# Optimization experiments

Hardware: AMD Instinct MI355X
Metric: run time of the kernel (lower is better)

Reference implementation:

```python
import math
import jax, jax.numpy as jnp
import numpy as np

L, D, H, DF, V, T, B = 4, 1024, 16, 4096, 32000, 2048, 1
HD = D // H
EPS = 1e-5

def _ln(x, w, b):
    m = jnp.mean(x, -1, keepdims=True)
    v = jnp.mean((x - m) ** 2, -1, keepdims=True)
    return (x - m) * jax.lax.rsqrt(v + EPS) * w + b

def setup_inputs() -> dict:
    key = jax.random.key(0)
    ks = jax.random.split(key, 8)
    s = 0.02
    return {
        'ids':   jax.random.randint(ks[0], (B, T), 0, V),
        'te':    jax.random.normal(ks[1], (V, D), jnp.float32) * s,
        'pe':    jax.random.normal(ks[2], (T, D), jnp.float32) * s,
        'qkv_w': jax.random.normal(ks[3], (L, D, 3 * D), jnp.float32) * s,
        'qkv_b': jnp.zeros((L, 3 * D), jnp.float32),
        'out_w': jax.random.normal(ks[4], (L, D, D), jnp.float32) * s,
        'out_b': jnp.zeros((L, D), jnp.float32),
        'ln1_w': jnp.ones((L, D), jnp.float32),
        'ln1_b': jnp.zeros((L, D), jnp.float32),
        'ln2_w': jnp.ones((L, D), jnp.float32),
        'ln2_b': jnp.zeros((L, D), jnp.float32),
        'up_w':  jax.random.normal(ks[5], (L, D, DF), jnp.float32) * s,
        'up_b':  jnp.zeros((L, DF), jnp.float32),
        'dn_w':  jax.random.normal(ks[6], (L, DF, D), jnp.float32) * s,
        'dn_b':  jnp.zeros((L, D), jnp.float32),
        'lnf_w': jnp.ones((D,), jnp.float32),
        'lnf_b': jnp.zeros((D,), jnp.float32),
    }

def reference(ids, te, pe, qkv_w, qkv_b, out_w, out_b, ln1_w, ln1_b,
              ln2_w, ln2_b, up_w, up_b, dn_w, dn_b, lnf_w, lnf_b):
    b, t = ids.shape
    x = te[ids] + pe[:t][None]                        # [b,t,D]
    causal = jnp.tril(jnp.ones((t, t), bool))          # [t,t]
    scale = 1.0 / math.sqrt(HD)
    for i in range(L):
        h = _ln(x, ln1_w[i], ln1_b[i])
        qkv = (h @ qkv_w[i] + qkv_b[i]).reshape(b, t, 3, H, HD)
        q, k, v = qkv[:, :, 0], qkv[:, :, 1], qkv[:, :, 2]
        sc = jnp.einsum('bqhd,bkhd->bhqk', q, k) * scale
        sc = jnp.where(causal, sc, -jnp.inf)
        att = jax.nn.softmax(sc, axis=-1)
        ao = jnp.einsum('bhqk,bkhd->bqhd', att, v).reshape(b, t, D)
        x = x + ao @ out_w[i] + out_b[i]
        h = _ln(x, ln2_w[i], ln2_b[i])
        x = x + jax.nn.silu(h @ up_w[i] + up_b[i]) @ dn_w[i] + dn_b[i]
    x = _ln(x, lnf_w, lnf_b)
    logits = x @ te.T                                  # tied head, no bias
    return logits
```

## Files before the change

kernel.cpp:

```cpp
#include <hip/hip_runtime.h>

typedef __attribute__((ext_vector_type(8))) short short8;
typedef __attribute__((ext_vector_type(4))) short short4v;
typedef __attribute__((ext_vector_type(4))) float f32x4;
typedef unsigned short u16;

#define Lc 4
#define Dc 1024
#define Hc 16
#define HDc 64
#define DFc 4096
#define Vc 32000
#define Tc 2048

__device__ __forceinline__ u16 f2bf(float f) {
  union { float f; unsigned u; } v; v.f = f;
  return (u16)((v.u + 0x7FFFu + ((v.u >> 16) & 1u)) >> 16);
}

__device__ __forceinline__ void gload_lds16(const u16* g, u16* l) {
  __builtin_amdgcn_global_load_lds(
      (const __attribute__((address_space(1))) unsigned int*)(g),
      (__attribute__((address_space(3))) unsigned int*)(l), 16, 0, 0);
}

#define BARS do { __builtin_amdgcn_s_barrier(); __builtin_amdgcn_sched_barrier(0); } while (0)
#define LGKM0 do { asm volatile("s_waitcnt lgkmcnt(0)" ::: "memory"); __builtin_amdgcn_sched_barrier(0); } while (0)
#define VMC(n) do { asm volatile("s_waitcnt vmcnt(" #n ")" ::: "memory"); __builtin_amdgcn_sched_barrier(0); } while (0)

__global__ __launch_bounds__(256) void castk(const float* __restrict__ in, u16* __restrict__ out) {
  size_t i = ((size_t)blockIdx.x * 256 + threadIdx.x) * 4;
  float4 v = *(const float4*)(in + i);
  short4v o; o[0] = f2bf(v.x); o[1] = f2bf(v.y); o[2] = f2bf(v.z); o[3] = f2bf(v.w);
  *(short4v*)(out + i) = o;
}

__global__ __launch_bounds__(256) void embedln(const int* __restrict__ ids, const float* __restrict__ te,
                                               const float* __restrict__ pe, const float* __restrict__ w,
                                               const float* __restrict__ b, float* __restrict__ x,
                                               u16* __restrict__ out) {
  int t = blockIdx.x, tid = threadIdx.x;
  int id = ids[t];
  float4 a = *(const float4*)(te + (size_t)id * Dc + tid * 4);
  float4 p = *(const float4*)(pe + (size_t)t * Dc + tid * 4);
  float4 v; v.x = a.x + p.x; v.y = a.y + p.y; v.z = a.z + p.z; v.w = a.w + p.w;
  size_t i = (size_t)t * Dc + tid * 4;
  *(float4*)(x + i) = v;
  float s = v.x + v.y + v.z + v.w;
  float q = v.x * v.x + v.y * v.y + v.z * v.z + v.w * v.w;
  #pragma unroll
  for (int off = 1; off < 64; off <<= 1) { s += __shfl_xor(s, off); q += __shfl_xor(q, off); }
  __shared__ float red[8];
  if ((tid & 63) == 0) { red[tid >> 6] = s; red[4 + (tid >> 6)] = q; }
  __syncthreads();
  s = red[0] + red[1] + red[2] + red[3];
  q = red[4] + red[5] + red[6] + red[7];
  float mean = s * (1.0f / Dc);
  float rstd = rsqrtf(q * (1.0f / Dc) - mean * mean + 1e-5f);
  float4 wv = *(const float4*)(w + tid * 4);
  float4 bv = *(const float4*)(b + tid * 4);
  out[i + 0] = f2bf((v.x - mean) * rstd * wv.x + bv.x);
  out[i + 1] = f2bf((v.y - mean) * rstd * wv.y + bv.y);
  out[i + 2] = f2bf((v.z - mean) * rstd * wv.z + bv.z);
  out[i + 3] = f2bf((v.w - mean) * rstd * wv.w + bv.w);
}

template<int SK>
__global__ __launch_bounds__(256) void combineln(float* __restrict__ x, const float* __restrict__ p,
                                                 const float* __restrict__ bias, const float* __restrict__ w,
                                                 const float* __restrict__ b, u16* __restrict__ out) {
  int t = blockIdx.x, tid = threadIdx.x;
  size_t i = (size_t)t * Dc + tid * 4;
  float4 v = *(const float4*)(x + i);
  #pragma unroll
  for (int s = 0; s < SK; s++) {
    float4 q2 = *(const float4*)(p + (size_t)s * Tc * Dc + i);
    v.x += q2.x; v.y += q2.y; v.z += q2.z; v.w += q2.w;
  }
  float4 bb = *(const float4*)(bias + tid * 4);
  v.x += bb.x; v.y += bb.y; v.z += bb.z; v.w += bb.w;
  *(float4*)(x + i) = v;
  float s = v.x + v.y + v.z + v.w;
  float q = v.x * v.x + v.y * v.y + v.z * v.z + v.w * v.w;
  #pragma unroll
  for (int off = 1; off < 64; off <<= 1) { s += __shfl_xor(s, off); q += __shfl_xor(q, off); }
  __shared__ float red[8];
  if ((tid & 63) == 0) { red[tid >> 6] = s; red[4 + (tid >> 6)] = q; }
  __syncthreads();
  s = red[0] + red[1] + red[2] + red[3];
  q = red[4] + red[5] + red[6] + red[7];
  float mean = s * (1.0f / Dc);
  float rstd = rsqrtf(q * (1.0f / Dc) - mean * mean + 1e-5f);
  float4 wv = *(const float4*)(w + tid * 4);
  float4 bv = *(const float4*)(b + tid * 4);
  out[i + 0] = f2bf((v.x - mean) * rstd * wv.x + bv.x);
  out[i + 1] = f2bf((v.y - mean) * rstd * wv.y + bv.y);
  out[i + 2] = f2bf((v.z - mean) * rstd * wv.z + bv.z);
  out[i + 3] = f2bf((v.w - mean) * rstd * wv.w + bv.w);
}

__global__ __launch_bounds__(256) void transpose4(const float* __restrict__ qw, const float* __restrict__ ow,
                                                  const float* __restrict__ uw, const float* __restrict__ dw,
                                                  u16* __restrict__ qT, u16* __restrict__ oT,
                                                  u16* __restrict__ uT, u16* __restrict__ dT) {
  __shared__ float tl[32][33];
  int id = blockIdx.x;
  const float* in; u16* out; int R, C, t;
  if (id < 3072)      { in = qw; out = qT; R = Dc;  C = 3 * Dc; t = id; }
  else if (id < 4096) { in = ow; out = oT; R = Dc;  C = Dc;     t = id - 3072; }
  else if (id < 8192) { in = uw; out = uT; R = Dc;  C = DFc;    t = id - 4096; }
  else                { in = dw; out = dT; R = DFc; C = Dc;     t = id - 8192; }
  int tilesX = C >> 5;
  int c0 = (t % tilesX) * 32, r0 = (t / tilesX) * 32;
  int lx = threadIdx.x & 31, ly = threadIdx.x >> 5;
  #pragma unroll
  for (int i = ly; i < 32; i += 8) tl[i][lx] = in[(size_t)(r0 + i) * C + c0 + lx];
  __syncthreads();
  #pragma unroll
  for (int i = ly; i < 32; i += 8) out[(size_t)(c0 + i) * R + r0 + lx] = f2bf(tl[lx][i]);
}

template<int EPI>
__global__ __launch_bounds__(256) void gemm128m(
    const u16* __restrict__ A, const u16* __restrict__ Bt, const float* __restrict__ bias,
    u16* __restrict__ outb, float* __restrict__ outf, int M, int N, int K, int KS) {
  __shared__ __align__(16) u16 lds[32768];
  u16* As = lds;
  u16* Bs = lds + 16384;
  const int NK = KS >> 6;

  int tid = threadIdx.x;
  int w = tid >> 6, lane = tid & 63;
  int lr = lane & 15, lg = lane >> 4;
  int wr = w >> 1, wc = w & 1;

  int m0 = blockIdx.y * 128, n0 = blockIdx.x * 128;
  int kbase = blockIdx.z * KS;

  int offg[4];
  #pragma unroll
  for (int j = 0; j < 4; j++) {
    int p = tid + j * 256;
    int row = p >> 3;
    int uc = (p & 7) ^ (row & 7);
    offg[j] = row * K + uc * 8;
  }
  const u16* aB = A + (size_t)m0 * K + kbase;
  const u16* bB = Bt + (size_t)n0 * K + kbase;

  auto stA = [&](int kt) {
    u16* l = As + ((kt & 1) << 13) + w * 512;
    #pragma unroll
    for (int j = 0; j < 4; j++)
      gload_lds16(aB + kt * 64 + offg[j], l + j * 2048);
  };
  auto stB = [&](int kt) {
    u16* l = Bs + ((kt & 1) << 13) + w * 512;
    #pragma unroll
    for (int j = 0; j < 4; j++)
      gload_lds16(bB + kt * 64 + offg[j], l + j * 2048);
  };

  int colx0 = ((0 * 4 + lg) ^ (lr & 7)) * 8;
  int colx1 = ((1 * 4 + lg) ^ (lr & 7)) * 8;
  int abase = (wr * 64 + lr) * 64;
  int bbase = (wc * 64 + lr) * 64;

  f32x4 acc[4][4] = {};

  stB(0); stA(0); stB(1);
  VMC(4);
  BARS;

  for (int kt = 0; kt < NK; ++kt) {
    const u16* sA = As + ((kt & 1) << 13);
    const u16* sB = Bs + ((kt & 1) << 13);
    short8 af[4][2], bf[4][2];

    #pragma unroll
    for (int m = 0; m < 2; m++) {
      af[m][0] = *(const short8*)(sA + abase + m * 1024 + colx0);
      af[m][1] = *(const short8*)(sA + abase + m * 1024 + colx1);
    }
    #pragma unroll
    for (int n = 0; n < 4; n++) {
      bf[n][0] = *(const short8*)(sB + bbase + n * 1024 + colx0);
      bf[n][1] = *(const short8*)(sB + bbase + n * 1024 + colx1);
    }
    if (kt + 1 < NK) stA(kt + 1);
    BARS;
    LGKM0;
    __builtin_amdgcn_s_setprio(1);
    #pragma unroll
    for (int m = 0; m < 2; m++)
      #pragma unroll
      for (int n = 0; n < 4; n++)
        #pragma unroll
        for (int ks = 0; ks < 2; ks++)
          acc[m][n] = __builtin_amdgcn_mfma_f32_16x16x32_bf16(af[m][ks], bf[n][ks], acc[m][n], 0, 0, 0);
    __builtin_amdgcn_s_setprio(0);
    BARS;

    #pragma unroll
    for (int m = 2; m < 4; m++) {
      af[m][0] = *(const short8*)(sA + abase + m * 1024 + colx0);
      af[m][1] = *(const short8*)(sA + abase + m * 1024 + colx1);
    }
    if (kt + 2 < NK) { stB(kt + 2); VMC(4); }
    else if (kt + 1 < NK) { VMC(0); }
    BARS;
    LGKM0;
    __builtin_amdgcn_s_setprio(1);
    #pragma unroll
    for (int m = 2; m < 4; m++)
      #pragma unroll
      for (int n = 0; n < 4; n++)
        #pragma unroll
        for (int ks = 0; ks < 2; ks++)
          acc[m][n] = __builtin_amdgcn_mfma_f32_16x16x32_bf16(af[m][ks], bf[n][ks], acc[m][n], 0, 0, 0);
    __builtin_amdgcn_s_setprio(0);
    BARS;
  }

  float* op = outf + (EPI == 4 ? (size_t)blockIdx.z * M * N : 0);
  u16* vtp = (u16*)outf;
  #pragma unroll
  for (int n = 0; n < 4; n++) {
    int gn = n0 + wc * 64 + n * 16 + lr;
    float bv = (EPI == 0 || EPI == 1 || EPI == 5) ? bias[gn] : 0.0f;
    #pragma unroll
    for (int m = 0; m < 4; m++) {
      if (EPI == 5 && gn >= 2 * Dc) {
        int gmb = m0 + wr * 64 + m * 16 + lg * 4;
        short4v o;
        #pragma unroll
        for (int r = 0; r < 4; r++) o[r] = (short)f2bf(acc[m][n][r] + bv);
        *(short4v*)(vtp + (size_t)(gn - 2 * Dc) * Tc + gmb) = o;
      } else {
        #pragma unroll
        for (int r = 0; r < 4; r++) {
          int gm = m0 + wr * 64 + m * 16 + lg * 4 + r;
          float v = acc[m][n][r] + bv;
          size_t idx = (size_t)gm * N + gn;
          if (EPI == 0 || EPI == 5) outb[idx] = f2bf(v);
          else if (EPI == 1) outb[idx] = f2bf(v / (1.0f + __expf(-v)));
          else op[idx] = v;
        }
      }
    }
  }
}

__global__ __launch_bounds__(512) void gemm256(const u16* __restrict__ A, const u16* __restrict__ Bt,
                                               float* __restrict__ outf, int M, int N, int K) {
  __shared__ __align__(16) u16 lds[65536];
  u16* AsU = lds;
  u16* BsU = lds + 32768;
  const int NK = K >> 6;

  int tid = threadIdx.x;
  int w = tid >> 6, lane = tid & 63;
  int lr = lane & 15, lg = lane >> 4;
  int wr = w >> 2, wc = w & 3;

  int flat = blockIdx.y * gridDim.x + blockIdx.x;
  {
    int nwg = gridDim.x * gridDim.y;
    int q = nwg >> 3, r = nwg & 7, xc = flat & 7, s = flat >> 3;
    flat = (xc < r ? xc * (q + 1) : r * (q + 1) + (xc - r) * q) + s;
  }
  int bm = flat % gridDim.x, bn = flat / gridDim.x;
  int m0 = bm * 256, n0 = bn * 256;

  int row0 = tid >> 3;
  int uc0 = (tid & 7) ^ (row0 & 7);
  int offg = row0 * K + uc0 * 8;
  const u16* aB = A + (size_t)m0 * K;
  const u16* bB = Bt + (size_t)n0 * K;

  auto stA = [&](int kt, int half) {
    const u16* g = aB + (size_t)half * 128 * K + kt * 64 + offg;
    u16* l = AsU + (((kt & 1) * 2 + half) << 13) + w * 512;
    gload_lds16(g, l);
    gload_lds16(g + 64 * K, l + 4096);
  };
  auto stB = [&](int kt, int half) {
    const u16* g = bB + (size_t)half * 128 * K + kt * 64 + offg;
    u16* l = BsU + (((kt & 1) * 2 + half) << 13) + w * 512;
    gload_lds16(g, l);
    gload_lds16(g + 64 * K, l + 4096);
  };

  int colx0 = ((0 * 4 + lg) ^ (lr & 7)) * 8;
  int colx1 = ((1 * 4 + lg) ^ (lr & 7)) * 8;
  int arow = lr * 64;
  int brow = ((wc & 1) * 64 + lr) * 64;

  f32x4 acc[8][4] = {};

  stB(0, 0); stB(0, 1); stA(0, 0); stA(0, 1); stB(1, 0); stB(1, 1);
  VMC(4);
  BARS;

  for (int kt = 0; kt < NK; ++kt) {
    int slot = kt & 1;
    const u16* sA = AsU + ((slot * 2 + wr) << 13);
    const u16* sB = BsU + ((slot * 2 + (wc >> 1)) << 13);
    short8 af0[4][2], af1[4][2], bf0[2][2], bf1[2][2];

    #pragma unroll
    for (int m = 0; m < 4; m++) {
      af0[m][0] = *(const short8*)(sA + arow + m * 1024 + colx0);
      af0[m][1] = *(const short8*)(sA + arow + m * 1024 + colx1);
    }
    #pragma unroll
    for (int n = 0; n < 2; n++) {
      bf0[n][0] = *(const short8*)(sB + brow + n * 1024 + colx0);
      bf0[n][1] = *(const short8*)(sB + brow + n * 1024 + colx1);
      bf1[n][0] = *(const short8*)(sB + brow + (n + 2) * 1024 + colx0);
      bf1[n][1] = *(const short8*)(sB + brow + (n + 2) * 1024 + colx1);
    }
    if (kt + 1 < NK) { stA(kt + 1, 0); stA(kt + 1, 1); }
    BARS;
    LGKM0;
    __builtin_amdgcn_s_setprio(1);
    #pragma unroll
    for (int m = 0; m < 4; m++)
      #pragma unroll
      for (int n = 0; n < 2; n++)
        #pragma unroll
        for (int ks = 0; ks < 2; ks++)
          acc[m][n] = __builtin_amdgcn_mfma_f32_16x16x32_bf16(af0[m][ks], bf0[n][ks], acc[m][n], 0, 0, 0);
    #pragma unroll
    for (int m = 0; m < 4; m++)
      #pragma unroll
      for (int n = 0; n < 2; n++)
        #pragma unroll
        for (int ks = 0; ks < 2; ks++)
          acc[m][n + 2] = __builtin_amdgcn_mfma_f32_16x16x32_bf16(af0[m][ks], bf1[n][ks], acc[m][n + 2], 0, 0, 0);
    __builtin_amdgcn_s_setprio(0);
    BARS;

    #pragma unroll
    for (int m = 0; m < 4; m++) {
      af1[m][0] = *(const short8*)(sA + arow + (m + 4) * 1024 + colx0);
      af1[m][1] = *(const short8*)(sA + arow + (m + 4) * 1024 + colx1);
    }
    if (kt + 2 < NK) { stB(kt + 2, 0); stB(kt + 2, 1); VMC(4); }
    else if (kt + 1 < NK) { VMC(0); }
    BARS;
    LGKM0;
    __builtin_amdgcn_s_setprio(1);
    #pragma unroll
    for (int m = 0; m < 4; m++)
      #pragma unroll
      for (int n = 0; n < 2; n++)
        #pragma unroll
        for (int ks = 0; ks < 2; ks++)
          acc[m + 4][n] = __builtin_amdgcn_mfma_f32_16x16x32_bf16(af1[m][ks], bf0[n][ks], acc[m + 4][n], 0, 0, 0);
    #pragma unroll
    for (int m = 0; m < 4; m++)
      #pragma unroll
      for (int n = 0; n < 2; n++)
        #pragma unroll
        for (int ks = 0; ks < 2; ks++)
          acc[m + 4][n + 2] = __builtin_amdgcn_mfma_f32_16x16x32_bf16(af1[m][ks], bf1[n][ks], acc[m + 4][n + 2], 0, 0, 0);
    __builtin_amdgcn_s_setprio(0);
    BARS;
  }

  #pragma unroll
  for (int m = 0; m < 8; m++) {
    #pragma unroll
    for (int n = 0; n < 4; n++) {
      int gn = n0 + wc * 64 + n * 16 + lr;
      #pragma unroll
      for (int r = 0; r < 4; r++) {
        int gm = m0 + wr * 128 + m * 16 + lg * 4 + r;
        outf[(size_t)gm * N + gn] = acc[m][n][r];
      }
    }
  }
}

__global__ __launch_bounds__(512) void attnk(const u16* __restrict__ qkv, const u16* __restrict__ vt,
                                             u16* __restrict__ ao) {
  __shared__ u16 Plds[8][16][72];
  __shared__ float Cacc[4][64][16];
  __shared__ float Cl[4][64][4];
  int bid = blockIdx.x;
  int hh = bid >> 5;
  int qb = (bid & 256) ? (31 - (bid & 31)) : (bid & 31);
  int tid = threadIdx.x, l = tid & 63, w = tid >> 6;
  int w4 = w & 3, ishi = w >> 2;
  int lr = l & 15, lg = l >> 4;
  int qr0 = qb * 64 + w4 * 16;
  const u16* qbase = qkv + (size_t)(qr0 + lr) * (3 * Dc) + hh * HDc + lg * 8;
  short8 aq0 = *(const short8*)qbase;
  short8 aq1 = *(const short8*)(qbase + 32);
  f32x4 acco[4] = {};
  float rs[4] = {0.0f, 0.0f, 0.0f, 0.0f};
  int nkb = (qr0 + 79) >> 6;
  int half = nkb >> 1;
  int klo = ishi ? half : 0;
  int khi = ishi ? nkb : half;
  const float cl2 = 0.125f * 1.44269504088896f;
  for (int kb = klo; kb < khi; kb++) {
    int kk0 = kb * 64;
    float sv[4][4];
    bool msk = (kb == nkb - 1);
    #pragma unroll
    for (int st = 0; st < 4; st++) {
      int kt0 = kk0 + st * 16;
      const u16* kbase = qkv + (size_t)(kt0 + lr) * (3 * Dc) + Dc + hh * HDc + lg * 8;
      short8 bk0 = *(const short8*)kbase;
      short8 bk1 = *(const short8*)(kbase + 32);
      f32x4 s = {};
      s = __builtin_amdgcn_mfma_f32_16x16x32_bf16(aq0, bk0, s, 0, 0, 0);
      s = __builtin_amdgcn_mfma_f32_16x16x32_bf16(aq1, bk1, s, 0, 0, 0);
      if (msk) {
        int gcol = kt0 + lr;
        #pragma unroll
        for (int r = 0; r < 4; r++) {
          int grow = qr0 + lg * 4 + r;
          sv[st][r] = (gcol <= grow) ? s[r] * cl2 : -__builtin_inff();
        }
      } else {
        #pragma unroll
        for (int r = 0; r < 4; r++) sv[st][r] = s[r] * cl2;
      }
    }
    #pragma unroll
    for (int st = 0; st < 4; st++) {
      #pragma unroll
      for (int r = 0; r < 4; r++) {
        float p = __builtin_amdgcn_exp2f(fminf(sv[st][r], 45.0f));
        sv[st][r] = p;
        rs[r] += p;
      }
    }
    #pragma unroll
    for (int st = 0; st < 4; st++) {
      #pragma unroll
      for (int r = 0; r < 4; r++) Plds[w][lg * 4 + r][st * 16 + lr] = f2bf(sv[st][r]);
    }
    short8 pa0 = *(const short8*)&Plds[w][lr][lg * 8];
    short8 pa1 = *(const short8*)&Plds[w][lr][32 + lg * 8];
    #pragma unroll
    for (int nt = 0; nt < 4; nt++) {
      const u16* vbase = vt + (size_t)(hh * HDc + nt * 16 + lr) * Tc + kk0 + lg * 8;
      short8 bv0 = *(const short8*)vbase;
      short8 bv1 = *(const short8*)(vbase + 32);
      acco[nt] = __builtin_amdgcn_mfma_f32_16x16x32_bf16(pa0, bv0, acco[nt], 0, 0, 0);
      acco[nt] = __builtin_amdgcn_mfma_f32_16x16x32_bf16(pa1, bv1, acco[nt], 0, 0, 0);
    }
  }
  #pragma unroll
  for (int off = 1; off < 16; off <<= 1) {
    #pragma unroll
    for (int r = 0; r < 4; r++) rs[r] += __shfl_xor(rs[r], off);
  }
  if (ishi) {
    #pragma unroll
    for (int nt = 0; nt < 4; nt++)
      #pragma unroll
      for (int r = 0; r < 4; r++) Cacc[w4][l][nt * 4 + r] = acco[nt][r];
    #pragma unroll
    for (int r = 0; r < 4; r++) Cl[w4][l][r] = rs[r];
  }
  __syncthreads();
  if (!ishi) {
    float linv[4];
    #pragma unroll
    for (int r = 0; r < 4; r++) linv[r] = 1.0f / (rs[r] + Cl[w4][l][r]);
    #pragma unroll
    for (int nt = 0; nt < 4; nt++) {
      #pragma unroll
      for (int r = 0; r < 4; r++) {
        float val = (acco[nt][r] + Cacc[w4][l][nt * 4 + r]) * linv[r];
        ao[(size_t)(qr0 + lg * 4 + r) * Dc + hh * HDc + nt * 16 + lr] = f2bf(val);
      }
    }
  }
}

extern "C" void kernel_launch(void* const* d_in, const int* in_sizes, int n_in,
                              void* d_out, int out_size, void* d_ws, size_t ws_size,
                              hipStream_t stream) {
  const int*   ids   = (const int*)d_in[0];
  const float* te    = (const float*)d_in[1];
  const float* pe    = (const float*)d_in[2];
  const float* qkv_w = (const float*)d_in[3];
  const float* qkv_b = (const float*)d_in[4];
  const float* out_w = (const float*)d_in[5];
  const float* out_b = (const float*)d_in[6];
  const float* ln1_w = (const float*)d_in[7];
  const float* ln1_b = (const float*)d_in[8];
  const float* ln2_w = (const float*)d_in[9];
  const float* ln2_b = (const float*)d_in[10];
  const float* up_w  = (const float*)d_in[11];
  const float* up_b  = (const float*)d_in[12];
  const float* dn_w  = (const float*)d_in[13];
  const float* dn_b  = (const float*)d_in[14];
  const float* lnf_w = (const float*)d_in[15];
  const float* lnf_b = (const float*)d_in[16];
  float* logits = (float*)d_out;

  char* ws = (char*)d_ws;
  size_t off = 0;
  auto alloc = [&](size_t bytes) { void* p = ws + off; off += (bytes + 255) & ~(size_t)255; return p; };
  float* x    = (float*)alloc((size_t)Tc * Dc * 4);
  u16* hbuf   = (u16*)alloc((size_t)Tc * Dc * 2);
  u16* qkvb   = (u16*)alloc((size_t)Tc * 3 * Dc * 2);
  u16* aob    = (u16*)alloc((size_t)Tc * Dc * 2);
  u16* ubuf   = (u16*)alloc((size_t)Tc * DFc * 2);
  u16* vtb    = (u16*)alloc((size_t)Dc * Tc * 2);
  u16* tebf   = (u16*)alloc((size_t)Vc * Dc * 2);
  u16* qkvT   = (u16*)alloc((size_t)3 * Dc * Dc * 2);
  u16* outT   = (u16*)alloc((size_t)Dc * Dc * 2);
  u16* upT    = (u16*)alloc((size_t)DFc * Dc * 2);
  u16* dnT    = (u16*)alloc((size_t)Dc * DFc * 2);
  float* pbuf = (float*)alloc((size_t)4 * Tc * Dc * 4);

  castk<<<Vc * Dc / 1024, 256, 0, stream>>>(te, tebf);
  embedln<<<Tc, 256, 0, stream>>>(ids, te, pe, ln1_w, ln1_b, x, hbuf);

  for (int i = 0; i < Lc; i++) {
    transpose4<<<12288, 256, 0, stream>>>(
        qkv_w + (size_t)i * Dc * 3 * Dc, out_w + (size_t)i * Dc * Dc,
        up_w + (size_t)i * Dc * DFc, dn_w + (size_t)i * DFc * Dc,
        qkvT, outT, upT, dnT);

    gemm128m<5><<<dim3(3 * Dc / 128, Tc / 128, 1), 256, 0, stream>>>(
        hbuf, qkvT, qkv_b + (size_t)i * 3 * Dc, qkvb, (float*)vtb, Tc, 3 * Dc, Dc, Dc);
    attnk<<<512, 512, 0, stream>>>(qkvb, vtb, aob);
    gemm128m<4><<<dim3(Dc / 128, Tc / 128, 2), 256, 0, stream>>>(
        aob, outT, nullptr, nullptr, pbuf, Tc, Dc, Dc, Dc / 2);
    combineln<2><<<Tc, 256, 0, stream>>>(x, pbuf, out_b + (size_t)i * Dc,
                                         ln2_w + (size_t)i * Dc, ln2_b + (size_t)i * Dc, hbuf);
    gemm128m<1><<<dim3(DFc / 128, Tc / 128, 1), 256, 0, stream>>>(
        hbuf, upT, up_b + (size_t)i * DFc, ubuf, nullptr, Tc, DFc, Dc, Dc);
    gemm128m<4><<<dim3(Dc / 128, Tc / 128, 4), 256, 0, stream>>>(
        ubuf, dnT, nullptr, nullptr, pbuf, Tc, Dc, DFc, DFc / 4);
    if (i < Lc - 1)
      combineln<4><<<Tc, 256, 0, stream>>>(x, pbuf, dn_b + (size_t)i * Dc,
                                           ln1_w + (size_t)(i + 1) * Dc, ln1_b + (size_t)(i + 1) * Dc, hbuf);
    else
      combineln<4><<<Tc, 256, 0, stream>>>(x, pbuf, dn_b + (size_t)i * Dc, lnf_w, lnf_b, hbuf);
  }

  gemm256<<<dim3(Tc / 256, Vc / 256), 512, 0, stream>>>(hbuf, tebf, logits, Tc, Vc, Dc);
}
```

Baseline: 938.7 us.

## Prefetch LDS fragments across phases and stage logits epilogue through LDS

```diff
diff --git a/kernel.cpp b/kernel.cpp
--- a/kernel.cpp
+++ b/kernel.cpp
@@ -25,7 +25,7 @@
 }
 
 #define BARS do { __builtin_amdgcn_s_barrier(); __builtin_amdgcn_sched_barrier(0); } while (0)
-#define LGKM0 do { asm volatile("s_waitcnt lgkmcnt(0)" ::: "memory"); __builtin_amdgcn_sched_barrier(0); } while (0)
+#define LGKM(n) do { asm volatile("s_waitcnt lgkmcnt(" #n ")" ::: "memory"); __builtin_amdgcn_sched_barrier(0); } while (0)
 #define VMC(n) do { asm volatile("s_waitcnt vmcnt(" #n ")" ::: "memory"); __builtin_amdgcn_sched_barrier(0); } while (0)
 
 __global__ __launch_bounds__(256) void castk(const float* __restrict__ in, u16* __restrict__ out) {
@@ -189,7 +189,7 @@
     }
     if (kt + 1 < NK) stA(kt + 1);
     BARS;
-    LGKM0;
+    LGKM(0);
     __builtin_amdgcn_s_setprio(1);
     #pragma unroll
     for (int m = 0; m < 2; m++)
@@ -209,7 +209,7 @@
     if (kt + 2 < NK) { stB(kt + 2); VMC(4); }
     else if (kt + 1 < NK) { VMC(0); }
     BARS;
-    LGKM0;
+    LGKM(0);
     __builtin_amdgcn_s_setprio(1);
     #pragma unroll
     for (int m = 2; m < 4; m++)
@@ -296,23 +296,26 @@
   int arow = lr * 64;
   int brow = ((wc & 1) * 64 + lr) * 64;
 
-  f32x4 acc[8][4] = {};
-
-  stB(0, 0); stB(0, 1); stA(0, 0); stA(0, 1); stB(1, 0); stB(1, 1);
-  VMC(4);
-  BARS;
-
-  for (int kt = 0; kt < NK; ++kt) {
-    int slot = kt & 1;
+  short8 af0[4][2], af1[4][2], bf0[2][2], bf1[2][2];
+
+  auto rd_af_lo = [&](int slot) {
     const u16* sA = AsU + ((slot * 2 + wr) << 13);
-    const u16* sB = BsU + ((slot * 2 + (wc >> 1)) << 13);
-    short8 af0[4][2], af1[4][2], bf0[2][2], bf1[2][2];
-
     #pragma unroll
     for (int m = 0; m < 4; m++) {
       af0[m][0] = *(const short8*)(sA + arow + m * 1024 + colx0);
       af0[m][1] = *(const short8*)(sA + arow + m * 1024 + colx1);
     }
+  };
+  auto rd_af_hi = [&](int slot) {
+    const u16* sA = AsU + ((slot * 2 + wr) << 13);
+    #pragma unroll
+    for (int m = 0; m < 4; m++) {
+      af1[m][0] = *(const short8*)(sA + arow + (m + 4) * 1024 + colx0);
+      af1[m][1] = *(const short8*)(sA + arow + (m + 4) * 1024 + colx1);
+    }
+  };
+  auto rd_bf = [&](int slot) {
+    const u16* sB = BsU + ((slot * 2 + (wc >> 1)) << 13);
     #pragma unroll
     for (int n = 0; n < 2; n++) {
       bf0[n][0] = *(const short8*)(sB + brow + n * 1024 + colx0);
@@ -320,9 +323,22 @@
       bf1[n][0] = *(const short8*)(sB + brow + (n + 2) * 1024 + colx0);
       bf1[n][1] = *(const short8*)(sB + brow + (n + 2) * 1024 + colx1);
     }
+  };
+
+  f32x4 acc[8][4] = {};
+
+  stB(0, 0); stB(0, 1); stA(0, 0); stA(0, 1); stB(1, 0); stB(1, 1);
+  VMC(4);
+  BARS;
+  rd_af_lo(0);
+
+  for (int kt = 0; kt < NK; ++kt) {
+    int slot = kt & 1;
+    rd_bf(slot);
+    rd_af_hi(slot);
+    LGKM(8);
+    BARS;
     if (kt + 1 < NK) { stA(kt + 1, 0); stA(kt + 1, 1); }
-    BARS;
-    LGKM0;
     __builtin_amdgcn_s_setprio(1);
     #pragma unroll
     for (int m = 0; m < 4; m++)
@@ -339,17 +355,15 @@
         for (int ks = 0; ks < 2; ks++)
           acc[m][n + 2] = __builtin_amdgcn_mfma_f32_16x16x32_bf16(af0[m][ks], bf1[n][ks], acc[m][n + 2], 0, 0, 0);
     __builtin_amdgcn_s_setprio(0);
-    BARS;
-
-    #pragma unroll
-    for (int m = 0; m < 4; m++) {
-      af1[m][0] = *(const short8*)(sA + arow + (m + 4) * 1024 + colx0);
-      af1[m][1] = *(const short8*)(sA + arow + (m + 4) * 1024 + colx1);
-    }
     if (kt + 2 < NK) { stB(kt + 2, 0); stB(kt + 2, 1); VMC(4); }
     else if (kt + 1 < NK) { VMC(0); }
     BARS;
-    LGKM0;
+    if (kt + 1 < NK) {
+      rd_af_lo((kt + 1) & 1);
+      LGKM(8);
+    } else {
+      LGKM(0);
+    }
     __builtin_amdgcn_s_setprio(1);
     #pragma unroll
     for (int m = 0; m < 4; m++)
@@ -366,18 +380,34 @@
         for (int ks = 0; ks < 2; ks++)
           acc[m + 4][n + 2] = __builtin_amdgcn_mfma_f32_16x16x32_bf16(af1[m][ks], bf1[n][ks], acc[m + 4][n + 2], 0, 0, 0);
     __builtin_amdgcn_s_setprio(0);
-    BARS;
-  }
-
-  #pragma unroll
-  for (int m = 0; m < 8; m++) {
-    #pragma unroll
-    for (int n = 0; n < 4; n++) {
-      int gn = n0 + wc * 64 + n * 16 + lr;
-      #pragma unroll
-      for (int r = 0; r < 4; r++) {
-        int gm = m0 + wr * 128 + m * 16 + lg * 4 + r;
-        outf[(size_t)gm * N + gn] = acc[m][n][r];
+  }
+
+  {
+    float* lf = (float*)lds;
+    #pragma unroll
+    for (int pass = 0; pass < 2; pass++) {
+      BARS;
+      if (wr == pass) {
+        #pragma unroll
+        for (int n = 0; n < 4; n++) {
+          int col = wc * 64 + n * 16 + lr;
+          #pragma unroll
+          for (int m = 0; m < 8; m++)
+            #pragma unroll
+            for (int r = 0; r < 4; r++) {
+              int rl = m * 16 + lg * 4 + r;
+              lf[rl * 256 + (col ^ (((rl >> 2) & 1) << 4))] = acc[m][n][r];
+            }
+        }
+      }
+      BARS;
+      #pragma unroll
+      for (int j = 0; j < 16; j++) {
+        int i4 = j * 2048 + tid * 4;
+        int row = i4 >> 8;
+        int col4 = i4 & 255;
+        f32x4 v = *(const f32x4*)(lf + row * 256 + (col4 ^ (((row >> 2) & 1) << 4)));
+        *(f32x4*)(outf + (size_t)(m0 + pass * 128 + row) * N + n0 + col4) = v;
       }
     }
   }
```

New measurement: 933.2 us. About the same (-0.6%).
